# Kernel tuning notes

Hardware: AMD Instinct MI355X
Metric: run time of the kernel (lower is better)

The kernel has to match this reference:

```python
import jax, jax.numpy as jnp
import numpy as np

B, L, D = 1, 2048, 768
H, DH = 12, 64  # n_heads, d_head (D // H)
LN_EPS = 1e-5
DEN_EPS = 1e-6


def setup_inputs() -> dict:
    key = jax.random.key(0)
    ks = jax.random.split(key, 11)
    s = 0.02
    return {
        "x": jax.random.normal(ks[0], (B, L, D), dtype=jnp.float32),
        "W_qkv": jax.random.normal(ks[1], (D, 3 * D), dtype=jnp.float32) * s,
        "b_qkv": jnp.zeros((3 * D,), dtype=jnp.float32),
        "W_sem": jax.random.normal(ks[2], (D, 2 * D), dtype=jnp.float32) * s,
        "b_sem": jnp.zeros((2 * D,), dtype=jnp.float32),
        "W_ctx": jax.random.normal(ks[3], (D, 2 * D), dtype=jnp.float32) * s,
        "b_ctx": jnp.zeros((2 * D,), dtype=jnp.float32),
        "W_proj": jax.random.normal(ks[4], (D, D), dtype=jnp.float32) * s,
        "b_proj": jnp.zeros((D,), dtype=jnp.float32),
        "ln_g": jnp.ones((D,), dtype=jnp.float32),
        "ln_b": jnp.zeros((D,), dtype=jnp.float32),
    }


def _heads(t):
    # [B,L,D] -> [B,H,L,DH]
    return t.reshape(B, L, H, DH).transpose(0, 2, 1, 3)


def reference(x, W_qkv, b_qkv, W_sem, b_sem, W_ctx, b_ctx, W_proj, b_proj, ln_g, ln_b):
    # LayerNorm
    mu = jnp.mean(x, axis=-1, keepdims=True)
    var = jnp.mean(jnp.square(x - mu), axis=-1, keepdims=True)
    x_norm = (x - mu) * jax.lax.rsqrt(var + LN_EPS) * ln_g + ln_b

    qkv = x_norm @ W_qkv + b_qkv
    q, k, v = jnp.split(qkv, 3, axis=-1)

    # interference gate from raw x
    sem = x @ W_sem + b_sem
    sem_amp = jax.nn.softplus(sem[..., :D])
    sem_phase = sem[..., D:]
    ctx = x @ W_ctx + b_ctx
    ctx_amp = jax.nn.softplus(ctx[..., :D])
    ctx_phase = ctx[..., D:]
    gate = jax.nn.sigmoid(sem_amp * ctx_amp * jnp.cos(sem_phase - ctx_phase))
    k = k * gate

    q_f = jax.nn.elu(_heads(q)) + 1.0  # [B,H,L,DH]
    k_f = jax.nn.elu(_heads(k)) + 1.0
    v_f = _heads(v)

    # causal linear attention: cumsum of kv outer products along L
    kv = jnp.einsum("bhld,bhle->bhlde", k_f, v_f)  # [B,H,L,DH,DH]
    kv_cum = jnp.cumsum(kv, axis=2)
    out_num = jnp.einsum("bhld,bhlde->bhle", q_f, kv_cum)  # [B,H,L,DH]

    k_cum = jnp.cumsum(k_f, axis=2)
    out_den = jnp.sum(q_f * k_cum, axis=-1, keepdims=True) + DEN_EPS

    attn = (out_num / out_den).transpose(0, 2, 1, 3).reshape(B, L, D)
    return attn @ W_proj + b_proj
```

## Files before the change

### kernel.cpp

```cpp
#include <hip/hip_runtime.h>
#include <math.h>

#define LSEQ 2048
#define DMODEL 768
#define NHEAD 12
#define DHEAD 64
#define NCHUNK 32
#define NMERGED 5376

typedef unsigned short ushort_t;
typedef __attribute__((ext_vector_type(8))) short short8;
typedef float float4v __attribute__((ext_vector_type(4)));

__device__ __forceinline__ ushort_t f2b(float f) {
    union { float f; unsigned int u; } v; v.f = f;
    unsigned int u = v.u;
    return (ushort_t)((u + 0x7fffu + ((u >> 16) & 1u)) >> 16);
}
__device__ __forceinline__ float b2f(ushort_t u) {
    union { unsigned int u; float f; } v; v.u = ((unsigned int)u) << 16;
    return v.f;
}

__device__ __forceinline__ void gl_lds16(const ushort_t* g, ushort_t* l) {
    __builtin_amdgcn_global_load_lds(
        (const __attribute__((address_space(1))) unsigned int*)g,
        (__attribute__((address_space(3))) unsigned int*)l, 16, 0, 0);
}

__global__ void pre_kernel(const float* __restrict__ x, const float* __restrict__ g,
                           const float* __restrict__ beta, ushort_t* __restrict__ xn,
                           ushort_t* __restrict__ xb,
                           const float* __restrict__ Wq, const float* __restrict__ Ws,
                           const float* __restrict__ Wc, ushort_t* __restrict__ Tm,
                           const float* __restrict__ Wp, ushort_t* __restrict__ Tp) {
    __shared__ float red[4];
    __shared__ float bc;
    __shared__ float tile[32][33];
    int tid = threadIdx.x;
    if (blockIdx.x < 2048) {
        int row = blockIdx.x;
        const float* xr = x + (size_t)row * DMODEL;
        float v0 = xr[tid], v1 = xr[tid + 256], v2 = xr[tid + 512];
        float s = v0 + v1 + v2;
#pragma unroll
        for (int o = 32; o > 0; o >>= 1) s += __shfl_down(s, o);
        if ((tid & 63) == 0) red[tid >> 6] = s;
        __syncthreads();
        if (tid == 0) bc = (red[0] + red[1] + red[2] + red[3]) * (1.0f / DMODEL);
        __syncthreads();
        float mu = bc;
        float d0 = v0 - mu, d1 = v1 - mu, d2 = v2 - mu;
        float vs = d0 * d0 + d1 * d1 + d2 * d2;
        __syncthreads();
#pragma unroll
        for (int o = 32; o > 0; o >>= 1) vs += __shfl_down(vs, o);
        if ((tid & 63) == 0) red[tid >> 6] = vs;
        __syncthreads();
        if (tid == 0) bc = rsqrtf((red[0] + red[1] + red[2] + red[3]) * (1.0f / DMODEL) + 1e-5f);
        __syncthreads();
        float r = bc;
        ushort_t* xo = xn + (size_t)row * DMODEL;
        ushort_t* xc = xb + (size_t)row * DMODEL;
        xo[tid]       = f2b(d0 * r * g[tid]       + beta[tid]);
        xo[tid + 256] = f2b(d1 * r * g[tid + 256] + beta[tid + 256]);
        xo[tid + 512] = f2b(d2 * r * g[tid + 512] + beta[tid + 512]);
        xc[tid]       = f2b(v0);
        xc[tid + 256] = f2b(v1);
        xc[tid + 512] = f2b(v2);
    } else {
        int bid = blockIdx.x - 2048;
        int nb = bid % 72;
        int kb = (bid / 72) % 24;
        int zb = bid / (72 * 24);
        const float* W; ushort_t* Wt; int N;
        switch (zb) {
            case 0: W = Wq; Wt = Tm;                        N = 2304; break;
            case 1: W = Ws; Wt = Tm + (size_t)2304 * 768;   N = 1536; break;
            case 2: W = Wc; Wt = Tm + (size_t)3840 * 768;   N = 1536; break;
            default: W = Wp; Wt = Tp;                       N = 768;  break;
        }
        int nbase = nb * 32;
        if (nbase >= N) return;
        int tr = tid >> 5, tc = tid & 31;
        int kbase = kb * 32;
#pragma unroll
        for (int p = 0; p < 4; p++) {
            int r = p * 8 + tr;
            tile[r][tc] = W[(size_t)(kbase + r) * N + nbase + tc];
        }
        __syncthreads();
#pragma unroll
        for (int p = 0; p < 4; p++) {
            int r = p * 8 + tr;
            Wt[(size_t)(nbase + r) * 768 + kbase + tc] = f2b(tile[tc][r]);
        }
    }
}

__global__ __launch_bounds__(256) void gemm_merged_kernel(
    const ushort_t* __restrict__ Axn, const ushort_t* __restrict__ Axb,
    const ushort_t* __restrict__ Bt,
    const float* __restrict__ b_qkv, const float* __restrict__ b_sem,
    const float* __restrict__ b_ctx, ushort_t* __restrict__ Cb,
    ushort_t* __restrict__ vb) {
    const int K = 768;
    __shared__ ushort_t As[128 * 64];
    __shared__ ushort_t Bs[128 * 64];
    int tid = threadIdx.x;
    int wave = tid >> 6, lane = tid & 63;
    int wm = (wave >> 1) * 64, wn = (wave & 1) * 64;
    int quad = lane >> 4, l16 = lane & 15;
    int bid = blockIdx.x;
    int xcd = bid & 7, slot = bid >> 3;
    int tile_id = xcd * 84 + slot;
    int m0 = (tile_id & 15) * 128;
    int n0 = (tile_id >> 4) * 128;
    const ushort_t* A = (n0 < 2304) ? Axn : Axb;
    const float* bias = (n0 < 2304) ? (b_qkv + n0) : (n0 < 3840 ? (b_sem + n0 - 2304) : (b_ctx + n0 - 3840));

    int rb = tid >> 3;
    int c8 = tid & 7;

    float4v acc[4][4];
#pragma unroll
    for (int i = 0; i < 4; i++)
#pragma unroll
        for (int j = 0; j < 4; j++)
#pragma unroll
            for (int r = 0; r < 4; r++) acc[i][j][r] = 0.0f;

    for (int k0 = 0; k0 < K; k0 += 64) {
#pragma unroll
        for (int p = 0; p < 4; p++) {
            int r = p * 32 + rb;
            int kc = (c8 ^ (r & 7)) * 8;
            gl_lds16(A  + (size_t)(m0 + r) * K + k0 + kc, &As[(p * 256 + wave * 64) * 8]);
            gl_lds16(Bt + (size_t)(n0 + r) * K + k0 + kc, &Bs[(p * 256 + wave * 64) * 8]);
        }
        __syncthreads();
#pragma unroll
        for (int ks = 0; ks < 2; ks++) {
            short8 af[4], bf[4];
#pragma unroll
            for (int i = 0; i < 4; i++) {
                int rr = wm + i * 16 + l16;
                af[i] = *(const short8*)&As[rr * 64 + (((ks * 4 + quad) ^ (rr & 7)) * 8)];
            }
#pragma unroll
            for (int j = 0; j < 4; j++) {
                int rr = wn + j * 16 + l16;
                bf[j] = *(const short8*)&Bs[rr * 64 + (((ks * 4 + quad) ^ (rr & 7)) * 8)];
            }
#pragma unroll
            for (int i = 0; i < 4; i++)
#pragma unroll
                for (int j = 0; j < 4; j++)
                    acc[i][j] = __builtin_amdgcn_mfma_f32_16x16x32_bf16(af[i], bf[j], acc[i][j], 0, 0, 0);
        }
        __syncthreads();
    }
    bool is_v = (n0 >= 1536 && n0 < 2304);
#pragma unroll
    for (int i = 0; i < 4; i++) {
#pragma unroll
        for (int j = 0; j < 4; j++) {
            int colb = wn + j * 16 + l16;
            float bv = bias[colb];
#pragma unroll
            for (int r = 0; r < 4; r++) {
                int row = m0 + wm + i * 16 + quad * 4 + r;
                ushort_t o = f2b(acc[i][j][r] + bv);
                if (is_v) {
                    vb[(size_t)row * DMODEL + (n0 - 1536) + colb] = o;
                } else {
                    Cb[(size_t)row * NMERGED + n0 + colb] = o;
                }
            }
        }
    }
}

__global__ __launch_bounds__(256) void gemm_64_kernel(
    const ushort_t* __restrict__ A, const ushort_t* __restrict__ Bt,
    const float* __restrict__ bias, float* __restrict__ C,
    int N, int K) {
    __shared__ ushort_t As[64 * 64];
    __shared__ ushort_t Bs[64 * 64];
    int tid = threadIdx.x;
    int wave = tid >> 6, lane = tid & 63;
    int wm = (wave >> 1) * 32, wn = (wave & 1) * 32;
    int quad = lane >> 4, l16 = lane & 15;
    int m0 = blockIdx.y * 64, n0 = blockIdx.x * 64;

    int rb = tid >> 3;
    int c8 = tid & 7;

    float4v acc[2][2];
#pragma unroll
    for (int i = 0; i < 2; i++)
#pragma unroll
        for (int j = 0; j < 2; j++)
#pragma unroll
            for (int r = 0; r < 4; r++) acc[i][j][r] = 0.0f;

    for (int k0 = 0; k0 < K; k0 += 64) {
#pragma unroll
        for (int p = 0; p < 2; p++) {
            int r = p * 32 + rb;
            int kc = (c8 ^ (r & 7)) * 8;
            gl_lds16(A  + (size_t)(m0 + r) * K + k0 + kc, &As[(p * 256 + wave * 64) * 8]);
            gl_lds16(Bt + (size_t)(n0 + r) * K + k0 + kc, &Bs[(p * 256 + wave * 64) * 8]);
        }
        __syncthreads();
#pragma unroll
        for (int ks = 0; ks < 2; ks++) {
            short8 af[2], bf[2];
#pragma unroll
            for (int i = 0; i < 2; i++) {
                int rr = wm + i * 16 + l16;
                af[i] = *(const short8*)&As[rr * 64 + (((ks * 4 + quad) ^ (rr & 7)) * 8)];
            }
#pragma unroll
            for (int j = 0; j < 2; j++) {
                int rr = wn + j * 16 + l16;
                bf[j] = *(const short8*)&Bs[rr * 64 + (((ks * 4 + quad) ^ (rr & 7)) * 8)];
            }
#pragma unroll
            for (int i = 0; i < 2; i++)
#pragma unroll
                for (int j = 0; j < 2; j++)
                    acc[i][j] = __builtin_amdgcn_mfma_f32_16x16x32_bf16(af[i], bf[j], acc[i][j], 0, 0, 0);
        }
        __syncthreads();
    }
#pragma unroll
    for (int i = 0; i < 2; i++) {
#pragma unroll
        for (int j = 0; j < 2; j++) {
            int col = n0 + wn + j * 16 + l16;
            float bv = bias[col];
#pragma unroll
            for (int r = 0; r < 4; r++) {
                int row = m0 + wm + i * 16 + quad * 4 + r;
                C[(size_t)row * N + col] = acc[i][j][r] + bv;
            }
        }
    }
}

__device__ __forceinline__ float softplus_f(float x) {
    return (x > 15.f) ? x : log1pf(expf(x));
}

__global__ void gate_feat_kernel(const ushort_t* __restrict__ qscb,
                                 ushort_t* __restrict__ qf, ushort_t* __restrict__ kf) {
    int t = blockIdx.x * 256 + threadIdx.x;
    int l = t / 192, d = (t - l * 192) * 4;
    size_t base = (size_t)l * NMERGED;
    ushort_t sa[4], sp[4], ca[4], cp[4], q[4], k[4];
    *(uint2*)sa = *(const uint2*)&qscb[base + 2304 + d];
    *(uint2*)sp = *(const uint2*)&qscb[base + 3072 + d];
    *(uint2*)ca = *(const uint2*)&qscb[base + 3840 + d];
    *(uint2*)cp = *(const uint2*)&qscb[base + 4608 + d];
    *(uint2*)q  = *(const uint2*)&qscb[base + d];
    *(uint2*)k  = *(const uint2*)&qscb[base + 768 + d];
    ushort_t qo[4], ko[4];
#pragma unroll
    for (int j = 0; j < 4; j++) {
        float amp = softplus_f(b2f(sa[j])) * softplus_f(b2f(ca[j]));
        float tt = amp * cosf(b2f(sp[j]) - b2f(cp[j]));
        float gate = 1.0f / (1.0f + expf(-tt));
        float kv = b2f(k[j]) * gate;
        float qv = b2f(q[j]);
        qo[j] = f2b((qv > 0.f) ? qv + 1.0f : expf(qv));
        ko[j] = f2b((kv > 0.f) ? kv + 1.0f : expf(kv));
    }
    size_t o = (size_t)l * DMODEL + d;
    *(uint2*)&qf[o] = *(uint2*)qo;
    *(uint2*)&kf[o] = *(uint2*)ko;
}

__global__ __launch_bounds__(256) void chunk_sum_mfma(const ushort_t* __restrict__ kf,
                                                      const ushort_t* __restrict__ vb,
                                                      float* __restrict__ S) {
    int h = blockIdx.x % NHEAD;
    int c = blockIdx.x / NHEAD;
    __shared__ ushort_t Kt[64 * 72];
    __shared__ ushort_t Vt[64 * 72];
    int tid = threadIdx.x;
    const size_t hb = (size_t)h * DHEAD;
#pragma unroll
    for (int it = 0; it < 4; it++) {
        int r = it * 16 + (tid >> 4);
        int cc = (tid & 15) * 4;
        int lg = c * 64 + r;
        ushort_t kt4[4], vt4[4];
        *(uint2*)kt4 = *(const uint2*)&kf[(size_t)lg * DMODEL + hb + cc];
        *(uint2*)vt4 = *(const uint2*)&vb[(size_t)lg * DMODEL + hb + cc];
#pragma unroll
        for (int i2 = 0; i2 < 4; i2++) {
            Kt[(cc + i2) * 72 + r] = kt4[i2];
            Vt[(cc + i2) * 72 + r] = vt4[i2];
        }
    }
    __syncthreads();
    int wave = tid >> 6, lane = tid & 63, quad = lane >> 4, l16 = lane & 15;
    int wm = wave * 16;
    float4v acc[4];
#pragma unroll
    for (int jt = 0; jt < 4; jt++)
#pragma unroll
        for (int r = 0; r < 4; r++) acc[jt][r] = 0.0f;
#pragma unroll
    for (int ks = 0; ks < 2; ks++) {
        short8 af = *(const short8*)&Kt[(wm + l16) * 72 + ks * 32 + quad * 8];
#pragma unroll
        for (int jt = 0; jt < 4; jt++) {
            short8 bf = *(const short8*)&Vt[(jt * 16 + l16) * 72 + ks * 32 + quad * 8];
            acc[jt] = __builtin_amdgcn_mfma_f32_16x16x32_bf16(af, bf, acc[jt], 0, 0, 0);
        }
    }
    float* Sp = S + (size_t)(h * NCHUNK + c) * 4160;
#pragma unroll
    for (int jt = 0; jt < 4; jt++) {
        float4 o;
        o.x = acc[jt][0]; o.y = acc[jt][1]; o.z = acc[jt][2]; o.w = acc[jt][3];
        *(float4*)&Sp[(jt * 16 + l16) * 64 + wm + quad * 4] = o;
    }
    if (tid < 64) {
        float s = 0.f;
#pragma unroll
        for (int g = 0; g < 8; g++) {
            short8 kv8 = *(const short8*)&Kt[tid * 72 + g * 8];
#pragma unroll
            for (int i2 = 0; i2 < 8; i2++) s += b2f(((ushort_t*)&kv8)[i2]);
        }
        Sp[4096 + tid] = s;
    }
}

__global__ void prefix_kernel(const float* __restrict__ S, ushort_t* __restrict__ Pb,
                              float* __restrict__ kpf) {
    int h = blockIdx.x;
    int i = blockIdx.y * 256 + threadIdx.x;
    if (i >= 4160) return;
    float v[NCHUNK];
    size_t base = (size_t)h * NCHUNK * 4160 + i;
#pragma unroll
    for (int c2 = 0; c2 < NCHUNK; c2++) v[c2] = S[base + (size_t)c2 * 4160];
    float run = 0.f;
    if (i < 4096) {
        size_t pb = (size_t)h * NCHUNK * 4096 + i;
#pragma unroll
        for (int c2 = 0; c2 < NCHUNK; c2++) {
            Pb[pb + (size_t)c2 * 4096] = f2b(run);
            run += v[c2];
        }
    } else {
        size_t kb = (size_t)h * NCHUNK * 64 + (i - 4096);
#pragma unroll
        for (int c2 = 0; c2 < NCHUNK; c2++) {
            kpf[kb + (size_t)c2 * 64] = run;
            run += v[c2];
        }
    }
}

__global__ __launch_bounds__(256) void attn_out_mfma(const ushort_t* __restrict__ qf,
                                                     const ushort_t* __restrict__ kf,
                                                     const ushort_t* __restrict__ vb,
                                                     const ushort_t* __restrict__ Pb,
                                                     const float* __restrict__ kpf,
                                                     ushort_t* __restrict__ attn) {
    int h = blockIdx.x % NHEAD;
    int c = blockIdx.x / NHEAD;
    __shared__ ushort_t Qs[64 * 72];
    __shared__ ushort_t Ks[64 * 72];
    __shared__ ushort_t Pt[64 * 72];
    __shared__ ushort_t Vt[64 * 72];
    __shared__ float Sc[64 * 68];
    __shared__ float kpl[64];
    __shared__ float denp[4][64];
    __shared__ float dnl[64];
    int tid = threadIdx.x;
    const size_t hb = (size_t)h * DHEAD;
    const size_t pcb = (size_t)(h * NCHUNK + c);
#pragma unroll
    for (int it = 0; it < 2; it++) {
        int chunk = it * 256 + tid;
        int r = chunk >> 3, c8 = (chunk & 7) * 8;
        int lg = c * 64 + r;
        *(uint4*)&Qs[r * 72 + c8] = *(const uint4*)&qf[(size_t)lg * DMODEL + hb + c8];
        *(uint4*)&Ks[r * 72 + c8] = *(const uint4*)&kf[(size_t)lg * DMODEL + hb + c8];
        *(uint4*)&Pt[r * 72 + c8] = *(const uint4*)&Pb[pcb * 4096 + r * 64 + c8];
    }
#pragma unroll
    for (int it = 0; it < 4; it++) {
        int r = it * 16 + (tid >> 4);
        int cc = (tid & 15) * 4;
        int lg = c * 64 + r;
        ushort_t vt4[4];
        *(uint2*)vt4 = *(const uint2*)&vb[(size_t)lg * DMODEL + hb + cc];
#pragma unroll
        for (int i2 = 0; i2 < 4; i2++) Vt[(cc + i2) * 72 + r] = vt4[i2];
    }
    if (tid < 64) kpl[tid] = kpf[pcb * 64 + tid];
    __syncthreads();
    int wave = tid >> 6, lane = tid & 63, quad = lane >> 4, l16 = lane & 15;
    int wm = wave * 16;
    float4v s_acc[4], n_acc[4];
#pragma unroll
    for (int jt = 0; jt < 4; jt++)
#pragma unroll
        for (int r = 0; r < 4; r++) { s_acc[jt][r] = 0.0f; n_acc[jt][r] = 0.0f; }
#pragma unroll
    for (int ks = 0; ks < 2; ks++) {
        short8 aq = *(const short8*)&Qs[(wm + l16) * 72 + ks * 32 + quad * 8];
#pragma unroll
        for (int jt = 0; jt < 4; jt++) {
            short8 bk = *(const short8*)&Ks[(jt * 16 + l16) * 72 + ks * 32 + quad * 8];
            short8 bp = *(const short8*)&Pt[(jt * 16 + l16) * 72 + ks * 32 + quad * 8];
            s_acc[jt] = __builtin_amdgcn_mfma_f32_16x16x32_bf16(aq, bk, s_acc[jt], 0, 0, 0);
            n_acc[jt] = __builtin_amdgcn_mfma_f32_16x16x32_bf16(aq, bp, n_acc[jt], 0, 0, 0);
        }
    }
#pragma unroll
    for (int jt = 0; jt < 4; jt++)
#pragma unroll
        for (int r = 0; r < 4; r++)
            Sc[(wm + quad * 4 + r) * 68 + jt * 16 + l16] = s_acc[jt][r];
    __syncthreads();
    {
        int l = tid & 63, part = tid >> 6;
        float s = 0.f;
#pragma unroll
        for (int jj = 0; jj < 16; jj++) {
            int j = part * 16 + jj;
            float v = Sc[l * 68 + j];
            s += (j <= l) ? v : 0.f;
        }
#pragma unroll
        for (int dd = 0; dd < 16; dd++) {
            int d = part * 16 + dd;
            s += b2f(Qs[l * 72 + d]) * kpl[d];
        }
        denp[part][l] = s;
    }
    __syncthreads();
    if (tid < 64) dnl[tid] = denp[0][tid] + denp[1][tid] + denp[2][tid] + denp[3][tid] + 1e-6f;
    __syncthreads();
#pragma unroll
    for (int ks = 0; ks < 2; ks++) {
        int m = wm + l16;
        float sv[8];
        *(float4*)&sv[0] = *(const float4*)&Sc[m * 68 + ks * 32 + quad * 8];
        *(float4*)&sv[4] = *(const float4*)&Sc[m * 68 + ks * 32 + quad * 8 + 4];
        ushort_t am[8];
#pragma unroll
        for (int i2 = 0; i2 < 8; i2++) {
            int j = ks * 32 + quad * 8 + i2;
            am[i2] = (j <= m) ? f2b(sv[i2]) : (ushort_t)0;
        }
        short8 af = *(short8*)am;
#pragma unroll
        for (int jt = 0; jt < 4; jt++) {
            short8 bv = *(const short8*)&Vt[(jt * 16 + l16) * 72 + ks * 32 + quad * 8];
            n_acc[jt] = __builtin_amdgcn_mfma_f32_16x16x32_bf16(af, bv, n_acc[jt], 0, 0, 0);
        }
    }
#pragma unroll
    for (int jt = 0; jt < 4; jt++) {
        int e = jt * 16 + l16;
#pragma unroll
        for (int r = 0; r < 4; r++) {
            int l = wm + quad * 4 + r;
            float o = n_acc[jt][r] / dnl[l];
            attn[(size_t)(c * 64 + l) * DMODEL + hb + e] = f2b(o);
        }
    }
}

extern "C" void kernel_launch(void* const* d_in, const int* in_sizes, int n_in,
                              void* d_out, int out_size, void* d_ws, size_t ws_size,
                              hipStream_t stream) {
    const float* x      = (const float*)d_in[0];
    const float* W_qkv  = (const float*)d_in[1];
    const float* b_qkv  = (const float*)d_in[2];
    const float* W_sem  = (const float*)d_in[3];
    const float* b_sem  = (const float*)d_in[4];
    const float* W_ctx  = (const float*)d_in[5];
    const float* b_ctx  = (const float*)d_in[6];
    const float* W_proj = (const float*)d_in[7];
    const float* b_proj = (const float*)d_in[8];
    const float* ln_g   = (const float*)d_in[9];
    const float* ln_b   = (const float*)d_in[10];
    float* out = (float*)d_out;
    float* ws  = (float*)d_ws;

    ushort_t* Wt_merged = (ushort_t*)(ws);
    ushort_t* Wt_proj   = (ushort_t*)(ws + 2064384);
    ushort_t* xb        = (ushort_t*)(ws + 2359296);
    ushort_t* xnb       = (ushort_t*)(ws + 3145728);
    ushort_t* qscb      = (ushort_t*)(ws + 3932160);
    ushort_t* vb        = (ushort_t*)(ws + 14942208);
    ushort_t* qf        = (ushort_t*)(ws + 2359296);
    ushort_t* kf        = (ushort_t*)(ws + 3145728);
    float*    S         = ws;
    ushort_t* Pb        = (ushort_t*)(ws + 3932160);
    float*    kpf       = ws + 4718592;
    ushort_t* attnb     = (ushort_t*)(ws);

    pre_kernel<<<2048 + 72 * 24 * 4, 256, 0, stream>>>(x, ln_g, ln_b, xnb, xb,
                                                       W_qkv, W_sem, W_ctx, Wt_merged,
                                                       W_proj, Wt_proj);

    gemm_merged_kernel<<<672, 256, 0, stream>>>(
        xnb, xb, Wt_merged, b_qkv, b_sem, b_ctx, qscb, vb);

    gate_feat_kernel<<<(LSEQ * DMODEL / 4) / 256, 256, 0, stream>>>(qscb, qf, kf);
    chunk_sum_mfma<<<NHEAD * NCHUNK, 256, 0, stream>>>(kf, vb, S);
    prefix_kernel<<<dim3(NHEAD, 17), 256, 0, stream>>>(S, Pb, kpf);
    attn_out_mfma<<<NHEAD * NCHUNK, 256, 0, stream>>>(qf, kf, vb, Pb, kpf, attnb);

    gemm_64_kernel<<<dim3(768 / 64, LSEQ / 64), 256, 0, stream>>>(attnb, Wt_proj, b_proj, out, 768, 768);
}
```

Before: 172.7 us.

## Halve GEMM K-tile, stage merged GEMM output through LDS, de-alias workspace buffers

```diff
diff --git a/kernel.cpp b/kernel.cpp
--- a/kernel.cpp
+++ b/kernel.cpp
@@ -105,8 +105,9 @@
     const float* __restrict__ b_ctx, ushort_t* __restrict__ Cb,
     ushort_t* __restrict__ vb) {
     const int K = 768;
-    __shared__ ushort_t As[128 * 64];
-    __shared__ ushort_t Bs[128 * 64];
+    __shared__ ushort_t As[128 * 32];
+    __shared__ ushort_t Bs[128 * 32];
+    __shared__ ushort_t Ct[128 * 132];
     int tid = threadIdx.x;
     int wave = tid >> 6, lane = tid & 63;
     int wm = (wave >> 1) * 64, wn = (wave & 1) * 64;
@@ -119,8 +120,16 @@
     const ushort_t* A = (n0 < 2304) ? Axn : Axb;
     const float* bias = (n0 < 2304) ? (b_qkv + n0) : (n0 < 3840 ? (b_sem + n0 - 2304) : (b_ctx + n0 - 3840));
 
-    int rb = tid >> 3;
-    int c8 = tid & 7;
+    int r0 = tid >> 2;
+    int kc = ((tid & 3) ^ ((r0 >> 1) & 3)) * 8;
+    const ushort_t* Ag0 = A + (size_t)(m0 + r0) * K + kc;
+    const ushort_t* Ag1 = A + (size_t)(m0 + 64 + r0) * K + kc;
+    const ushort_t* Bg0 = Bt + (size_t)(n0 + r0) * K + kc;
+    const ushort_t* Bg1 = Bt + (size_t)(n0 + 64 + r0) * K + kc;
+    ushort_t* Al0 = &As[(wave * 64) * 8];
+    ushort_t* Al1 = &As[(256 + wave * 64) * 8];
+    ushort_t* Bl0 = &Bs[(wave * 64) * 8];
+    ushort_t* Bl1 = &Bs[(256 + wave * 64) * 8];
 
     float4v acc[4][4];
 #pragma unroll
@@ -130,37 +139,30 @@
 #pragma unroll
             for (int r = 0; r < 4; r++) acc[i][j][r] = 0.0f;
 
-    for (int k0 = 0; k0 < K; k0 += 64) {
-#pragma unroll
-        for (int p = 0; p < 4; p++) {
-            int r = p * 32 + rb;
-            int kc = (c8 ^ (r & 7)) * 8;
-            gl_lds16(A  + (size_t)(m0 + r) * K + k0 + kc, &As[(p * 256 + wave * 64) * 8]);
-            gl_lds16(Bt + (size_t)(n0 + r) * K + k0 + kc, &Bs[(p * 256 + wave * 64) * 8]);
-        }
-        __syncthreads();
-#pragma unroll
-        for (int ks = 0; ks < 2; ks++) {
-            short8 af[4], bf[4];
-#pragma unroll
-            for (int i = 0; i < 4; i++) {
-                int rr = wm + i * 16 + l16;
-                af[i] = *(const short8*)&As[rr * 64 + (((ks * 4 + quad) ^ (rr & 7)) * 8)];
-            }
-#pragma unroll
-            for (int j = 0; j < 4; j++) {
-                int rr = wn + j * 16 + l16;
-                bf[j] = *(const short8*)&Bs[rr * 64 + (((ks * 4 + quad) ^ (rr & 7)) * 8)];
-            }
-#pragma unroll
-            for (int i = 0; i < 4; i++)
-#pragma unroll
-                for (int j = 0; j < 4; j++)
-                    acc[i][j] = __builtin_amdgcn_mfma_f32_16x16x32_bf16(af[i], bf[j], acc[i][j], 0, 0, 0);
-        }
-        __syncthreads();
-    }
-    bool is_v = (n0 >= 1536 && n0 < 2304);
+    for (int k0 = 0; k0 < K; k0 += 32) {
+        gl_lds16(Ag0 + k0, Al0);
+        gl_lds16(Ag1 + k0, Al1);
+        gl_lds16(Bg0 + k0, Bl0);
+        gl_lds16(Bg1 + k0, Bl1);
+        __syncthreads();
+        short8 af[4], bf[4];
+#pragma unroll
+        for (int i = 0; i < 4; i++) {
+            int rr = wm + i * 16 + l16;
+            af[i] = *(const short8*)&As[rr * 32 + ((quad ^ ((rr >> 1) & 3)) * 8)];
+        }
+#pragma unroll
+        for (int j = 0; j < 4; j++) {
+            int rr = wn + j * 16 + l16;
+            bf[j] = *(const short8*)&Bs[rr * 32 + ((quad ^ ((rr >> 1) & 3)) * 8)];
+        }
+#pragma unroll
+        for (int i = 0; i < 4; i++)
+#pragma unroll
+            for (int j = 0; j < 4; j++)
+                acc[i][j] = __builtin_amdgcn_mfma_f32_16x16x32_bf16(af[i], bf[j], acc[i][j], 0, 0, 0);
+        __syncthreads();
+    }
 #pragma unroll
     for (int i = 0; i < 4; i++) {
 #pragma unroll
@@ -169,14 +171,24 @@
             float bv = bias[colb];
 #pragma unroll
             for (int r = 0; r < 4; r++) {
-                int row = m0 + wm + i * 16 + quad * 4 + r;
-                ushort_t o = f2b(acc[i][j][r] + bv);
-                if (is_v) {
-                    vb[(size_t)row * DMODEL + (n0 - 1536) + colb] = o;
-                } else {
-                    Cb[(size_t)row * NMERGED + n0 + colb] = o;
-                }
+                int row = wm + i * 16 + quad * 4 + r;
+                Ct[row * 132 + colb] = f2b(acc[i][j][r] + bv);
             }
+        }
+    }
+    __syncthreads();
+    bool is_v = (n0 >= 1536 && n0 < 2304);
+    int rr0 = tid >> 4;
+    int cc0 = (tid & 15) * 8;
+#pragma unroll
+    for (int p = 0; p < 8; p++) {
+        int r = p * 16 + rr0;
+        uint4 vdat = *(const uint4*)&Ct[r * 132 + cc0];
+        int grow = m0 + r;
+        if (is_v) {
+            *(uint4*)&vb[(size_t)grow * DMODEL + (n0 - 1536) + cc0] = vdat;
+        } else {
+            *(uint4*)&Cb[(size_t)grow * NMERGED + n0 + cc0] = vdat;
         }
     }
 }
@@ -185,16 +197,20 @@
     const ushort_t* __restrict__ A, const ushort_t* __restrict__ Bt,
     const float* __restrict__ bias, float* __restrict__ C,
     int N, int K) {
-    __shared__ ushort_t As[64 * 64];
-    __shared__ ushort_t Bs[64 * 64];
+    __shared__ ushort_t As[64 * 32];
+    __shared__ ushort_t Bs[64 * 32];
     int tid = threadIdx.x;
     int wave = tid >> 6, lane = tid & 63;
     int wm = (wave >> 1) * 32, wn = (wave & 1) * 32;
     int quad = lane >> 4, l16 = lane & 15;
     int m0 = blockIdx.y * 64, n0 = blockIdx.x * 64;
 
-    int rb = tid >> 3;
-    int c8 = tid & 7;
+    int r0 = tid >> 2;
+    int kc = ((tid & 3) ^ ((r0 >> 1) & 3)) * 8;
+    const ushort_t* Ag = A + (size_t)(m0 + r0) * K + kc;
+    const ushort_t* Bg = Bt + (size_t)(n0 + r0) * K + kc;
+    ushort_t* Al = &As[(wave * 16) * 32];
+    ushort_t* Bl = &Bs[(wave * 16) * 32];
 
     float4v acc[2][2];
 #pragma unroll
@@ -204,34 +220,26 @@
 #pragma unroll
             for (int r = 0; r < 4; r++) acc[i][j][r] = 0.0f;
 
-    for (int k0 = 0; k0 < K; k0 += 64) {
-#pragma unroll
-        for (int p = 0; p < 2; p++) {
-            int r = p * 32 + rb;
-            int kc = (c8 ^ (r & 7)) * 8;
-            gl_lds16(A  + (size_t)(m0 + r) * K + k0 + kc, &As[(p * 256 + wave * 64) * 8]);
-            gl_lds16(Bt + (size_t)(n0 + r) * K + k0 + kc, &Bs[(p * 256 + wave * 64) * 8]);
-        }
-        __syncthreads();
-#pragma unroll
-        for (int ks = 0; ks < 2; ks++) {
-            short8 af[2], bf[2];
-#pragma unroll
-            for (int i = 0; i < 2; i++) {
-                int rr = wm + i * 16 + l16;
-                af[i] = *(const short8*)&As[rr * 64 + (((ks * 4 + quad) ^ (rr & 7)) * 8)];
-            }
-#pragma unroll
-            for (int j = 0; j < 2; j++) {
-                int rr = wn + j * 16 + l16;
-                bf[j] = *(const short8*)&Bs[rr * 64 + (((ks * 4 + quad) ^ (rr & 7)) * 8)];
-            }
-#pragma unroll
-            for (int i = 0; i < 2; i++)
-#pragma unroll
-                for (int j = 0; j < 2; j++)
-                    acc[i][j] = __builtin_amdgcn_mfma_f32_16x16x32_bf16(af[i], bf[j], acc[i][j], 0, 0, 0);
-        }
+    for (int k0 = 0; k0 < K; k0 += 32) {
+        gl_lds16(Ag + k0, Al);
+        gl_lds16(Bg + k0, Bl);
+        __syncthreads();
+        short8 af[2], bf[2];
+#pragma unroll
+        for (int i = 0; i < 2; i++) {
+            int rr = wm + i * 16 + l16;
+            af[i] = *(const short8*)&As[rr * 32 + ((quad ^ ((rr >> 1) & 3)) * 8)];
+        }
+#pragma unroll
+        for (int j = 0; j < 2; j++) {
+            int rr = wn + j * 16 + l16;
+            bf[j] = *(const short8*)&Bs[rr * 32 + ((quad ^ ((rr >> 1) & 3)) * 8)];
+        }
+#pragma unroll
+        for (int i = 0; i < 2; i++)
+#pragma unroll
+            for (int j = 0; j < 2; j++)
+                acc[i][j] = __builtin_amdgcn_mfma_f32_16x16x32_bf16(af[i], bf[j], acc[i][j], 0, 0, 0);
         __syncthreads();
     }
 #pragma unroll
@@ -503,13 +511,13 @@
     ushort_t* xb        = (ushort_t*)(ws + 2359296);
     ushort_t* xnb       = (ushort_t*)(ws + 3145728);
     ushort_t* qscb      = (ushort_t*)(ws + 3932160);
+    ushort_t* qf        = (ushort_t*)(ws + 9437184);
+    ushort_t* kf        = (ushort_t*)(ws + 10223616);
+    float*    S         = ws + 11010048;
+    ushort_t* attnb     = (ushort_t*)(ws + 12607488);
     ushort_t* vb        = (ushort_t*)(ws + 14942208);
-    ushort_t* qf        = (ushort_t*)(ws + 2359296);
-    ushort_t* kf        = (ushort_t*)(ws + 3145728);
-    float*    S         = ws;
-    ushort_t* Pb        = (ushort_t*)(ws + 3932160);
-    float*    kpf       = ws + 4718592;
-    ushort_t* attnb     = (ushort_t*)(ws);
+    ushort_t* Pb        = (ushort_t*)(ws + 16777216);
+    float*    kpf       = ws + 17563648;
 
     pre_kernel<<<2048 + 72 * 24 * 4, 256, 0, stream>>>(x, ln_g, ln_b, xnb, xb,
                                                        W_qkv, W_sem, W_ctx, Wt_merged,
```

Measured after the change: 157.2 us, median of 2. 1.1x faster.
